# Optimization experiments

Measured on AMD Instinct MI355X. Metric: run time of the kernel, lower is better.

## Reference

```python
import jax, jax.numpy as jnp
import numpy as np

NUM_GLOBAL_EXPERTS = 256
LOCAL_START = 64  # global experts [64, 128) live on this rank


def setup_inputs() -> dict:
    key = jax.random.key(0)
    k1, = jax.random.split(key, 1)
    num_local_experts = 64
    # Routing ids: ~4.2M tokens x topk=8, values are GLOBAL expert ids in [0, 256)
    topk_ids = jax.random.randint(k1, (33554432,), 0, NUM_GLOBAL_EXPERTS, dtype=jnp.int32)
    # expert_map: global -> local; -1 for experts not owned by this rank
    gid = jnp.arange(NUM_GLOBAL_EXPERTS, dtype=jnp.int32)
    expert_map = jnp.where(
        (gid >= LOCAL_START) & (gid < LOCAL_START + num_local_experts),
        gid - LOCAL_START,
        jnp.int32(-1),
    )
    return {"topk_ids": topk_ids, "num_local_experts": num_local_experts, "expert_map": expert_map}


def reference(topk_ids, num_local_experts, expert_map=None):
    n = num_local_experts  # static python int
    ids = topk_ids.reshape(-1)
    if expert_map is not None:
        # invalid ids (< 0) stay invalid; valid global ids are remapped to local space
        ids = jnp.where(ids >= 0, expert_map[jnp.clip(ids, 0)], jnp.int32(-1))
    # Route all invalid / out-of-range ids into an overflow bucket n, then drop it.
    valid = (ids >= 0) & (ids < n)
    bucket = jnp.where(valid, ids, jnp.int32(n))
    counts = jax.ops.segment_sum(
        jnp.ones_like(bucket, dtype=jnp.int32), bucket, num_segments=n + 1
    )
    return counts[:n].astype(jnp.int32)
```

## Files before the change

kernel.cpp:

```cpp
#include <hip/hip_runtime.h>

#define BLOCK   512
#define NBLK    512
#define NBINS   256
#define NWAVES  (BLOCK / 64)
#define UNROLL  4

__global__ __launch_bounds__(BLOCK) void hist_fused(const int* __restrict__ ids,
                                                    int N,
                                                    const int* __restrict__ emap,
                                                    int emap_n,
                                                    int* __restrict__ out,
                                                    int n_local) {
    __shared__ int hist[NWAVES * NBINS];
    __shared__ int lmap[NBINS];
    __shared__ int fold[NBINS];
    __shared__ int s_lo, s_cnt, s_ok;
    const int tid = threadIdx.x;

    if (tid == 0) { s_lo = 0x7FFFFFFF; s_cnt = 0; s_ok = 1; }
    for (int i = tid; i < NWAVES * NBINS; i += BLOCK) hist[i] = 0;
    __syncthreads();

    for (int g = tid; g < NBINS; g += BLOCK) {
        int m = (g < emap_n) ? emap[g] : -1;
        lmap[g] = m;
        if (m >= 0) { atomicMin(&s_lo, g); atomicAdd(&s_cnt, 1); }
    }
    __syncthreads();
    const int lo = s_lo;
    const unsigned cnt = (unsigned)s_cnt;
    for (int g = tid; g < NBINS; g += BLOCK) {
        int expect = (g >= lo && (unsigned)(g - lo) < cnt) ? (g - lo) : -1;
        if (lmap[g] != expect) s_ok = 0;
    }
    __syncthreads();
    const int affine = s_ok;

    int* h = &hist[(tid >> 6) * NBINS];

    const int4* __restrict__ ids4 = (const int4*)ids;
    const int n4      = N >> 2;
    const int chunk   = BLOCK * UNROLL;
    const int gstride = (int)gridDim.x * chunk;
    const int n4_full = (n4 / gstride) * gstride;

    if (affine) {
        for (int i = (int)blockIdx.x * chunk + tid; i < n4_full; i += gstride) {
            int4 v[UNROLL];
#pragma unroll
            for (int u = 0; u < UNROLL; ++u) v[u] = ids4[i + u * BLOCK];
#pragma unroll
            for (int u = 0; u < UNROLL; ++u) {
                unsigned a = (unsigned)(v[u].x - lo);
                unsigned b = (unsigned)(v[u].y - lo);
                unsigned c = (unsigned)(v[u].z - lo);
                unsigned d = (unsigned)(v[u].w - lo);
                if (a < cnt) atomicAdd(&h[a], 1);
                if (b < cnt) atomicAdd(&h[b], 1);
                if (c < cnt) atomicAdd(&h[c], 1);
                if (d < cnt) atomicAdd(&h[d], 1);
            }
        }
        for (int i = n4_full + (int)blockIdx.x * BLOCK + tid; i < n4;
             i += (int)gridDim.x * BLOCK) {
            int4 v = ids4[i];
            unsigned a = (unsigned)(v.x - lo), b = (unsigned)(v.y - lo);
            unsigned c = (unsigned)(v.z - lo), d = (unsigned)(v.w - lo);
            if (a < cnt) atomicAdd(&h[a], 1);
            if (b < cnt) atomicAdd(&h[b], 1);
            if (c < cnt) atomicAdd(&h[c], 1);
            if (d < cnt) atomicAdd(&h[d], 1);
        }
        if (blockIdx.x == 0) {
            for (int i = (n4 << 2) + tid; i < N; i += BLOCK) {
                unsigned a = (unsigned)(ids[i] - lo);
                if (a < cnt) atomicAdd(&h[a], 1);
            }
        }
    } else {
        for (int i = (int)blockIdx.x * chunk + tid; i < n4_full; i += gstride) {
            int4 v[UNROLL];
#pragma unroll
            for (int u = 0; u < UNROLL; ++u) v[u] = ids4[i + u * BLOCK];
#pragma unroll
            for (int u = 0; u < UNROLL; ++u) {
                int l0 = ((unsigned)v[u].x < NBINS) ? lmap[v[u].x] : -1;
                int l1 = ((unsigned)v[u].y < NBINS) ? lmap[v[u].y] : -1;
                int l2 = ((unsigned)v[u].z < NBINS) ? lmap[v[u].z] : -1;
                int l3 = ((unsigned)v[u].w < NBINS) ? lmap[v[u].w] : -1;
                if (l0 >= 0) atomicAdd(&h[l0], 1);
                if (l1 >= 0) atomicAdd(&h[l1], 1);
                if (l2 >= 0) atomicAdd(&h[l2], 1);
                if (l3 >= 0) atomicAdd(&h[l3], 1);
            }
        }
        for (int i = n4_full + (int)blockIdx.x * BLOCK + tid; i < n4;
             i += (int)gridDim.x * BLOCK) {
            int4 v = ids4[i];
            int l0 = ((unsigned)v.x < NBINS) ? lmap[v.x] : -1;
            int l1 = ((unsigned)v.y < NBINS) ? lmap[v.y] : -1;
            int l2 = ((unsigned)v.z < NBINS) ? lmap[v.z] : -1;
            int l3 = ((unsigned)v.w < NBINS) ? lmap[v.w] : -1;
            if (l0 >= 0) atomicAdd(&h[l0], 1);
            if (l1 >= 0) atomicAdd(&h[l1], 1);
            if (l2 >= 0) atomicAdd(&h[l2], 1);
            if (l3 >= 0) atomicAdd(&h[l3], 1);
        }
        if (blockIdx.x == 0) {
            for (int i = (n4 << 2) + tid; i < N; i += BLOCK) {
                int v = ids[i];
                int l = ((unsigned)v < NBINS) ? lmap[v] : -1;
                if (l >= 0) atomicAdd(&h[l], 1);
            }
        }
    }
    __syncthreads();

    for (int b = tid; b < n_local; b += BLOCK) {
        int s = 0;
#pragma unroll
        for (int w = 0; w < NWAVES; ++w) s += hist[w * NBINS + b];
        fold[b] = s;
    }
    __syncthreads();

    const int npair = n_local >> 1;
    for (int p = tid; p < npair; p += BLOCK) {
        unsigned long long v =
            (unsigned long long)(unsigned)fold[2 * p] |
            ((unsigned long long)(unsigned)fold[2 * p + 1] << 32);
        if (v) atomicAdd((unsigned long long*)out + p, v);
    }
    if ((n_local & 1) && tid == 0) {
        int s = fold[n_local - 1];
        if (s) atomicAdd(&out[n_local - 1], s);
    }
}

extern "C" void kernel_launch(void* const* d_in, const int* in_sizes, int n_in,
                              void* d_out, int out_size, void* d_ws, size_t ws_size,
                              hipStream_t stream) {
    const int* topk_ids   = (const int*)d_in[0];
    const int* expert_map = (const int*)d_in[2];
    const int N       = in_sizes[0];
    const int emap_n  = in_sizes[2];
    const int n_local = out_size;

    hipMemsetAsync(d_out, 0, (size_t)n_local * sizeof(int), stream);
    hist_fused<<<NBLK, BLOCK, 0, stream>>>(topk_ids, N, expert_map, emap_n,
                                           (int*)d_out, n_local);
}
```

Before: 197.0 us.

## Replace global atomics with per-block partials and last-block reduction

Each block now writes its per-bin counts to a workspace array of partials, and does not issue global atomics to the output. A counter atomic finds the last block to finish, and that block reduces all partials with wave shuffles and writes the final counts. Block size and grid size also change, to 256 threads and 2048 blocks. The cost is extra workspace traffic and a serial final reduction in a single block, in exchange for removing contention on the output atomics.

```diff
diff --git a/kernel.cpp b/kernel.cpp
--- a/kernel.cpp
+++ b/kernel.cpp
@@ -1,21 +1,24 @@
 #include <hip/hip_runtime.h>
 
-#define BLOCK   512
-#define NBLK    512
+#define BLOCK   256
+#define NBLK    2048
 #define NBINS   256
 #define NWAVES  (BLOCK / 64)
 #define UNROLL  4
+#define NB1     NBLK
 
 __global__ __launch_bounds__(BLOCK) void hist_fused(const int* __restrict__ ids,
                                                     int N,
                                                     const int* __restrict__ emap,
                                                     int emap_n,
+                                                    int* __restrict__ partials,
+                                                    unsigned* __restrict__ ctr,
                                                     int* __restrict__ out,
                                                     int n_local) {
     __shared__ int hist[NWAVES * NBINS];
     __shared__ int lmap[NBINS];
-    __shared__ int fold[NBINS];
     __shared__ int s_lo, s_cnt, s_ok;
+    __shared__ unsigned s_old;
     const int tid = threadIdx.x;
 
     if (tid == 0) { s_lo = 0x7FFFFFFF; s_cnt = 0; s_ok = 1; }
@@ -121,20 +124,28 @@
         int s = 0;
 #pragma unroll
         for (int w = 0; w < NWAVES; ++w) s += hist[w * NBINS + b];
-        fold[b] = s;
+        partials[b * NB1 + blockIdx.x] = s;
     }
+
+    __threadfence();
     __syncthreads();
+    if (tid == 0) s_old = atomicAdd(ctr, 1u);
+    __syncthreads();
+    if (s_old != (unsigned)(gridDim.x - 1)) return;
 
-    const int npair = n_local >> 1;
-    for (int p = tid; p < npair; p += BLOCK) {
-        unsigned long long v =
-            (unsigned long long)(unsigned)fold[2 * p] |
-            ((unsigned long long)(unsigned)fold[2 * p + 1] << 32);
-        if (v) atomicAdd((unsigned long long*)out + p, v);
-    }
-    if ((n_local & 1) && tid == 0) {
-        int s = fold[n_local - 1];
-        if (s) atomicAdd(&out[n_local - 1], s);
+    __threadfence();
+    const int wave = tid >> 6, lane = tid & 63;
+    for (int b = wave; b < n_local; b += NWAVES) {
+        const int4* p = (const int4*)&partials[b * NB1];
+        int s = 0;
+#pragma unroll 2
+        for (int j = lane; j < NB1 / 4; j += 64) {
+            int4 v = p[j];
+            s += v.x + v.y + v.z + v.w;
+        }
+#pragma unroll
+        for (int off = 32; off > 0; off >>= 1) s += __shfl_down(s, off, 64);
+        if (lane == 0) out[b] = s;
     }
 }
 
@@ -147,7 +158,10 @@
     const int emap_n  = in_sizes[2];
     const int n_local = out_size;
 
-    hipMemsetAsync(d_out, 0, (size_t)n_local * sizeof(int), stream);
+    unsigned* ctr = (unsigned*)d_ws;
+    int* partials = (int*)((char*)d_ws + 256);
+
+    hipMemsetAsync(ctr, 0, sizeof(unsigned), stream);
     hist_fused<<<NBLK, BLOCK, 0, stream>>>(topk_ids, N, expert_map, emap_n,
-                                           (int*)d_out, n_local);
+                                           partials, ctr, (int*)d_out, n_local);
 }
```

Result: slower. 525.6 us (+166.9%).
